# Kernel optimization log

Hardware: AMD Instinct MI355X
Metric: run time of the kernel (lower is better)

The kernel has to match this reference:

```python
import jax, jax.numpy as jnp
import numpy as np

B, N, D, H, E, FF = 4, 256, 256, 8, 32, 512
DK = D // H
SCALE = DK ** -0.5
NEG = -9.0e15


def _norm_mul(t, w, b, ms):
    # graph norm over node axis (dim=1)
    mean = jnp.mean(t, axis=1, keepdims=True)
    std = jnp.sqrt(jnp.mean((t - ms * mean) ** 2, axis=1, keepdims=True))
    return w * (t - ms * mean) / (std + 1e-6) + b


def _layer_norm(t, w, b):
    mu = jnp.mean(t, axis=-1, keepdims=True)
    var = jnp.mean((t - mu) ** 2, axis=-1, keepdims=True)
    return w * (t - mu) * jax.lax.rsqrt(var + 1e-5) + b


def _ffn(t, W1, b1, W2, b2):
    return jax.nn.gelu(t @ W1 + b1, approximate=False) @ W2 + b2


def _forward(x, edge_fea, attn_bias, params, adj, adj1, use_adj):
    (gn1_w, gn1_b, gn1_ms, ln1_w, ln1_b, Wq, bq, Wk, bk, Wv, bv,
     Wap, bap, Wep, bep, Wo, bo, Woe, gn2_w, gn2_b, gn2_ms,
     W1, b1, W2, b2, ln2_w, ln2_b, W1e, b1e, W2e, b2e) = params
    adj_f = adj.astype(x.dtype)
    adj1_f = adj1.astype(x.dtype)

    y = _norm_mul(x, gn1_w, gn1_b, gn1_ms)              # [B,N,D]
    e_n = _layer_norm(edge_fea, ln1_w, ln1_b)           # [B,N,N,E]

    q = (y @ Wq + bq).reshape(B, N, H, DK) * SCALE
    k = (y @ Wk + bk).reshape(B, N, H, DK)
    v = (y @ Wv + bv).reshape(B, N, H, DK)
    scores = jnp.einsum('bihd,bjhd->bhij', q, k)        # [B,H,N,N]
    if use_adj:
        scores = jnp.where(adj_f[:, None] > 0, scores, NEG) * adj_f[:, None]

    # global branch: multiplicative attn_bias then softmax
    x_long = jax.nn.softmax(scores * attn_bias, axis=-1)
    out_long = jnp.einsum('bhij,bjhd->bihd', x_long, v)

    # edge-feature fusion
    edge_bias = jnp.swapaxes(e_n @ Wep + bep, 1, 3)     # [B,H,N,N]
    x_proj = (jnp.swapaxes(scores, 1, 3) @ Wap + bap) * adj1_f[..., None]  # [B,N,N,E]
    e_attn = (e_n + x_proj) @ Woe                       # [B,N,N,E]

    # local branch: scores gated by edge bias and local adjacency
    x_local = jax.nn.softmax(scores * edge_bias * adj1_f[:, None], axis=-1)
    out_local = jnp.einsum('bhij,bjhd->bihd', x_local, v)

    attn_out = (out_local + out_long).reshape(B, N, D) @ Wo + bo

    x_out = x + attn_out
    x_out = x_out + _ffn(_norm_mul(x_out, gn2_w, gn2_b, gn2_ms), W1, b1, W2, b2)

    e1 = edge_fea + e_attn
    e_out = e1 + _ffn(_layer_norm(e1, ln2_w, ln2_b), W1e, b1e, W2e, b2e)
    return x_out, e_out


def setup_inputs() -> dict:
    key = jax.random.key(0)
    keys = list(jax.random.split(key, 32))

    def nk():
        return keys.pop()

    def w(shape, s=0.02):
        return jax.random.normal(nk(), shape, jnp.float32) * s

    inp = {}
    inp['x'] = jax.random.normal(nk(), (B, N, D), jnp.float32)
    inp['adj'] = jax.random.randint(nk(), (B, N, N), 0, 2).astype(jnp.int32)
    inp['adj1'] = (jax.random.uniform(nk(), (B, N, N)) < 0.15).astype(jnp.int32)
    inp['use_adj'] = 1
    inp['edge_fea'] = jax.random.normal(nk(), (B, N, N, E), jnp.float32)
    inp['attn_bias'] = jax.random.uniform(nk(), (B, H, N, N), jnp.float32)
    for nm, dim in [('gn1', D), ('gn2', D)]:
        inp[nm + '_w'] = jnp.ones((dim,), jnp.float32)
        inp[nm + '_b'] = jnp.zeros((dim,), jnp.float32)
        inp[nm + '_ms'] = jnp.ones((dim,), jnp.float32)
    for nm, dim in [('ln1', E), ('ln2', E)]:
        inp[nm + '_w'] = jnp.ones((dim,), jnp.float32)
        inp[nm + '_b'] = jnp.zeros((dim,), jnp.float32)
    inp['Wq'], inp['bq'] = w((D, D)), jnp.zeros((D,), jnp.float32)
    inp['Wk'], inp['bk'] = w((D, D)), jnp.zeros((D,), jnp.float32)
    inp['Wv'], inp['bv'] = w((D, D)), jnp.zeros((D,), jnp.float32)
    inp['Wap'], inp['bap'] = w((H, E)), jnp.zeros((E,), jnp.float32)
    inp['Wep'], inp['bep'] = w((E, H)), jnp.zeros((H,), jnp.float32)
    inp['Wo'], inp['bo'] = w((D, D)), jnp.zeros((D,), jnp.float32)
    inp['Woe'] = w((E, E))
    inp['W1'], inp['b1'] = w((D, FF)), jnp.zeros((FF,), jnp.float32)
    inp['W2'], inp['b2'] = w((FF, D)), jnp.zeros((D,), jnp.float32)
    inp['W1e'], inp['b1e'] = w((E, FF)), jnp.zeros((FF,), jnp.float32)
    inp['W2e'], inp['b2e'] = w((FF, E)), jnp.zeros((E,), jnp.float32)
    return inp


def reference(x, adj, adj1, use_adj, edge_fea, attn_bias,
              gn1_w, gn1_b, gn1_ms, gn2_w, gn2_b, gn2_ms,
              ln1_w, ln1_b, ln2_w, ln2_b,
              Wq, bq, Wk, bk, Wv, bv, Wap, bap, Wep, bep, Wo, bo, Woe,
              W1, b1, W2, b2, W1e, b1e, W2e, b2e):
    params = (gn1_w, gn1_b, gn1_ms, ln1_w, ln1_b, Wq, bq, Wk, bk, Wv, bv,
              Wap, bap, Wep, bep, Wo, bo, Woe, gn2_w, gn2_b, gn2_ms,
              W1, b1, W2, b2, ln2_w, ln2_b, W1e, b1e, W2e, b2e)
    return _forward(x, edge_fea, attn_bias, params, adj, adj1, use_adj)
```

## Files before the change

kernel.cpp:

```cpp
#include <hip/hip_runtime.h>
#include <math.h>

constexpr int B_ = 4, N_ = 256, D_ = 256, H_ = 8, E_ = 32, FF_ = 512, DK_ = 32;
constexpr float SCALE_ = 0.17677669529663687f;
constexpr float NEG_ = -9.0e15f;

typedef unsigned short u16;
typedef unsigned int u32;
typedef __attribute__((ext_vector_type(8))) short bf16x8;
typedef __attribute__((ext_vector_type(4))) float f32x4;
typedef __attribute__((ext_vector_type(8))) _Float16 f16x8;
typedef __attribute__((ext_vector_type(2))) _Float16 f16x2;
typedef __attribute__((ext_vector_type(2))) __fp16 fp16x2_raw;

__device__ __forceinline__ float gelu_fast(float x) {
  float u = x * x;
  float q = x * fmaf(-0.071354816272f, u, -1.5957691216057308f);
  float e = __expf(q);
  return x * __builtin_amdgcn_rcpf(1.f + e);
}

__device__ __forceinline__ f16x2 cvt_pk_f16(float a, float b) {
  union { fp16x2_raw i; f16x2 o; } u;
  u.i = __builtin_amdgcn_cvt_pkrtz(a, b);
  return u.o;
}

__device__ __forceinline__ f16x2 gelu_pk(f16x2 x) {
  const f16x2 C5 = {(_Float16)0.0199471f, (_Float16)0.0199471f};
  const f16x2 C3 = {(_Float16)-0.1329807f, (_Float16)-0.1329807f};
  const f16x2 C1 = {(_Float16)0.7978846f, (_Float16)0.7978846f};
  const f16x2 HALF = {(_Float16)0.5f, (_Float16)0.5f};
  const f16x2 ONE = {(_Float16)1.f, (_Float16)1.f};
  f16x2 w = x * x;
  f16x2 p = w * C5 + C3;
  p = w * p + C1;
  f16x2 t = x * p + ONE;
  f16x2 hx = x * HALF;
  return hx * t;
}

__device__ __forceinline__ u16 f2bf(float x) {
  union { float f; u32 u; } v; v.f = x;
  u32 r = v.u + 0x7fffu + ((v.u >> 16) & 1u);
  return (u16)(r >> 16);
}

__device__ __forceinline__ u32 pk2bf(float a, float b) {
  union { float f; u32 u; } x, y; x.f = a; y.f = b;
  u32 ra = (x.u + 0x7fffu + ((x.u >> 16) & 1u)) >> 16;
  u32 rb = (y.u + 0x7fffu + ((y.u >> 16) & 1u)) & 0xffff0000u;
  return ra | rb;
}

__device__ __forceinline__ float bf2f(u16 h) {
  union { u32 u; float f; } v; v.u = ((u32)h) << 16; return v.f;
}

__global__ __launch_bounds__(256) void front_kernel(
    const float* __restrict__ Wq, const float* __restrict__ Wk,
    const float* __restrict__ Wv, const float* __restrict__ Wo,
    const float* __restrict__ W1, const float* __restrict__ W2,
    const float* __restrict__ W1e, const float* __restrict__ W2e,
    const float* __restrict__ Woe, const float* __restrict__ Wap,
    const float* __restrict__ bap,
    u16* __restrict__ wxp, u16* __restrict__ w1p, u16* __restrict__ w2p,
    u16* __restrict__ woep, u16* __restrict__ wwp,
    const float* __restrict__ x, float2* __restrict__ part,
    const float* __restrict__ e_in, const float* __restrict__ lnw,
    const float* __restrict__ lnb, const float* __restrict__ Wep,
    const float* __restrict__ bep, const int* __restrict__ adj1,
    u16* __restrict__ e_nb, u16* __restrict__ eb16) {
  int bx = blockIdx.x;
  int tid = threadIdx.x;
  if (bx < 256) {
    int idx = bx * 256 + tid;
    const float* W;
    int rel, Nn, kcs, cmask;
    if (idx < 32768) {
      int m = idx >> 13;
      W = (m == 0) ? Wq : (m == 1) ? Wk : (m == 2) ? Wv : Wo;
      rel = idx & 8191; Nn = 256; kcs = 4; cmask = 15;
    } else if (idx < 49152) {
      W = W1; rel = idx - 32768; Nn = 512; kcs = 5; cmask = 31;
    } else {
      W = W2; rel = idx - 49152; Nn = 256; kcs = 4; cmask = 15;
    }
    int fr = rel >> 6, lane = rel & 63;
    int kc = fr >> kcs, ctt = fr & cmask;
    int krow = kc * 32 + ((lane >> 4) << 3);
    int col = ctt * 16 + (lane & 15);
    u16 out[8];
#pragma unroll
    for (int j = 0; j < 8; j++)
      out[j] = f2bf(W[(size_t)(krow + j) * Nn + col]);
    uint4* dst = (uint4*)(wxp + ((size_t)idx << 3));
    *dst = make_uint4(((u32)out[0]) | ((u32)out[1] << 16),
                      ((u32)out[2]) | ((u32)out[3] << 16),
                      ((u32)out[4]) | ((u32)out[5] << 16),
                      ((u32)out[6]) | ((u32)out[7] << 16));
  } else if (bx < 320) {
    int idx = (bx - 256) * 256 + tid;
    {
      int t = idx >> 9, rem = idx & 511, lane = rem >> 3, j = rem & 7;
      int k = ((lane >> 4) << 3) + j, col = (t << 4) + (lane & 15);
      w1p[idx] = f2bf(W1e[k * FF_ + col]);
    }
    {
      int f = idx >> 9, rem = idx & 511, lane = rem >> 3, j = rem & 7;
      int nc = f >> 2, kp = (f >> 1) & 1, ct = f & 1;
      int unit = nc * 64 + kp * 32 + 16 * (j >> 2) + 4 * (lane >> 4) + (j & 3);
      int col = ct * 16 + (lane & 15);
      union { _Float16 h; u16 u; } cv;
      cv.h = (_Float16)W2e[unit * E_ + col];
      w2p[idx] = cv.u;
    }
    if (idx < 1024) {
      int ct = idx >> 9, rem = idx & 511, lane = rem >> 3, j = rem & 7;
      int k = ((lane >> 4) << 3) + j, col = ct * 16 + (lane & 15);
      woep[idx] = f2bf(Woe[k * E_ + col]);
      float v = 0.f;
      if (k < 8) {
        for (int e = 0; e < 32; e++) v += Wap[k * E_ + e] * Woe[e * E_ + col];
      } else if (k == 8) {
        for (int e = 0; e < 32; e++) v += bap[e] * Woe[e * E_ + col];
      }
      wwp[idx] = f2bf(v);
    }
  } else if (bx < 448) {
    int i = bx - 320;
    int b = i & 3, by = (i >> 2) & 3, nz = i >> 4;
    int d = tid & 63, gn = tid >> 6;
    __shared__ float2 red[4][64];
    const float* xp = x + ((size_t)b * N_ * D_) + (size_t)(nz * 32 + gn * 8) * D_ + by * 64 + d;
    float s = 0.f, s2 = 0.f;
#pragma unroll
    for (int i2 = 0; i2 < 8; i2++) { float v = xp[(size_t)i2 * D_]; s += v; s2 += v * v; }
    red[gn][d] = make_float2(s, s2);
    __syncthreads();
    if (tid < 64) {
      float2 a = red[0][d], b2 = red[1][d], c = red[2][d], e = red[3][d];
      part[((b * 4 + by) * 8 + nz) * 64 + d] =
          make_float2(a.x + b2.x + c.x + e.x, a.y + b2.y + c.y + e.y);
    }
  } else {
    size_t t = (size_t)(bx - 448) * 256 + tid;
    int b = (int)(t >> 16), n2 = (int)((t >> 8) & 255), n1 = (int)(t & 255);
    size_t rowid = ((size_t)(b * N_ + n1)) * N_ + n2;
    const float4* ip = (const float4*)(e_in + rowid * E_);
    float4 v[8];
    float s = 0.f;
#pragma unroll
    for (int i = 0; i < 8; i++) { v[i] = ip[i]; s += v[i].x + v[i].y + v[i].z + v[i].w; }
    float mu = s * (1.f / E_);
    float q = 0.f;
#pragma unroll
    for (int i = 0; i < 8; i++) {
      float a = v[i].x - mu, b2 = v[i].y - mu, c = v[i].z - mu, dd = v[i].w - mu;
      q += a * a + b2 * b2 + c * c + dd * dd;
    }
    float inv = rsqrtf(q * (1.f / E_) + 1e-5f);
    float ov[32];
#pragma unroll
    for (int i = 0; i < 8; i++) {
      float4 wv = ((const float4*)lnw)[i];
      float4 bv = ((const float4*)lnb)[i];
      ov[4 * i + 0] = wv.x * (v[i].x - mu) * inv + bv.x;
      ov[4 * i + 1] = wv.y * (v[i].y - mu) * inv + bv.y;
      ov[4 * i + 2] = wv.z * (v[i].z - mu) * inv + bv.z;
      ov[4 * i + 3] = wv.w * (v[i].w - mu) * inv + bv.w;
    }
    u32 pk[16];
#pragma unroll
    for (int i = 0; i < 16; i++) pk[i] = pk2bf(ov[2 * i], ov[2 * i + 1]);
    uint4* op = (uint4*)(e_nb + rowid * E_);
    op[0] = make_uint4(pk[0], pk[1], pk[2], pk[3]);
    op[1] = make_uint4(pk[4], pk[5], pk[6], pk[7]);
    op[2] = make_uint4(pk[8], pk[9], pk[10], pk[11]);
    op[3] = make_uint4(pk[12], pk[13], pk[14], pk[15]);
    float acc[8];
#pragma unroll
    for (int h = 0; h < 8; h++) acc[h] = bep[h];
#pragma unroll
    for (int e = 0; e < 32; e++) {
      float re = ov[e];
#pragma unroll
      for (int h = 0; h < 8; h++) acc[h] = fmaf(re, Wep[e * 8 + h], acc[h]);
    }
    float a1f = (float)adj1[t];
#pragma unroll
    for (int h = 0; h < 8; h++)
      eb16[(((size_t)b * H_ + h) * N_ + n2) * N_ + n1] = f2bf(acc[h] * a1f);
  }
}

__global__ __launch_bounds__(256) void gnorm_part_kernel(
    const float* __restrict__ x, float2* __restrict__ part) {
  int b = blockIdx.x, by = blockIdx.y, nz = blockIdx.z;
  int tid = threadIdx.x, d = tid & 63, gn = tid >> 6;
  __shared__ float2 red[4][64];
  const float* xp = x + ((size_t)b * N_ * D_) + (size_t)(nz * 32 + gn * 8) * D_ + by * 64 + d;
  float s = 0.f, s2 = 0.f;
#pragma unroll
  for (int i = 0; i < 8; i++) { float v = xp[(size_t)i * D_]; s += v; s2 += v * v; }
  red[gn][d] = make_float2(s, s2);
  __syncthreads();
  if (tid < 64) {
    float2 a = red[0][d], b2 = red[1][d], c = red[2][d], e = red[3][d];
    part[((b * 4 + by) * 8 + nz) * 64 + d] =
        make_float2(a.x + b2.x + c.x + e.x, a.y + b2.y + c.y + e.y);
  }
}

__global__ __launch_bounds__(256) void gnorm_apply_kernel(
    const float* __restrict__ x, const float* __restrict__ w,
    const float* __restrict__ bw, const float* __restrict__ ms,
    const float2* __restrict__ part, float* __restrict__ out) {
  int b = blockIdx.x, by = blockIdx.y, nz = blockIdx.z;
  int tid = threadIdx.x, d = tid & 63, gn = tid >> 6;
  int d0 = by * 64;
  float s = 0.f, s2 = 0.f;
#pragma unroll
  for (int i = 0; i < 8; i++) {
    float2 p = part[((b * 4 + by) * 8 + i) * 64 + d];
    s += p.x; s2 += p.y;
  }
  float mean = s * (1.f / N_);
  float m2 = ms[d0 + d] * mean;
  float var = fmaxf(s2 * (1.f / N_) - 2.f * m2 * mean + m2 * m2, 0.f);
  float inv = 1.f / (sqrtf(var) + 1e-6f);
  float W = w[d0 + d], Bb = bw[d0 + d];
  const float* xp = x + ((size_t)b * N_ * D_) + (size_t)(nz * 32 + gn * 8) * D_ + d0 + d;
  float* op = out + ((size_t)b * N_ * D_) + (size_t)(nz * 32 + gn * 8) * D_ + d0 + d;
#pragma unroll
  for (int i = 0; i < 8; i++)
    op[(size_t)i * D_] = W * (xp[(size_t)i * D_] - m2) * inv + Bb;
}

template <int GELU>
__global__ __launch_bounds__(256) void mgemm_kernel(
    const float* __restrict__ A, const u16* __restrict__ Wp,
    const float* __restrict__ bias, const float* __restrict__ res,
    float* __restrict__ C, int K, int Nn, float scale) {
  int tid = threadIdx.x;
  int w = tid >> 6, l = tid & 63;
  int rt = w & 1, cts = (w >> 1) << 1;
  int row0 = blockIdx.y * 32, col0 = blockIdx.x * 64;
  int nf = Nn >> 4;
  f32x4 acc[2];
#pragma unroll
  for (int c2 = 0; c2 < 2; c2++) {
    float bb = bias[col0 + (cts + c2) * 16 + (l & 15)];
    acc[c2] = (f32x4){bb, bb, bb, bb};
  }
  int arow = row0 + rt * 16 + (l & 15);
  const float* ap = A + (size_t)arow * K + ((l >> 4) << 3);
  int nkc = K >> 5;
  for (int kc = 0; kc < nkc; kc++) {
    float4 a0 = *(const float4*)(ap + kc * 32);
    float4 a1 = *(const float4*)(ap + kc * 32 + 4);
    union { bf16x8 v; u32 u[4]; } af;
    af.u[0] = pk2bf(a0.x, a0.y); af.u[1] = pk2bf(a0.z, a0.w);
    af.u[2] = pk2bf(a1.x, a1.y); af.u[3] = pk2bf(a1.z, a1.w);
#pragma unroll
    for (int c2 = 0; c2 < 2; c2++) {
      bf16x8 wf = *(const bf16x8*)(Wp + (((size_t)kc * nf + (col0 >> 4) + cts + c2) << 9) + (l << 3));
      acc[c2] = __builtin_amdgcn_mfma_f32_16x16x32_bf16(af.v, wf, acc[c2], 0, 0, 0);
    }
  }
#pragma unroll
  for (int c2 = 0; c2 < 2; c2++) {
    int col = col0 + (cts + c2) * 16 + (l & 15);
#pragma unroll
    for (int rr = 0; rr < 4; rr++) {
      int row = row0 + rt * 16 + (l >> 4) * 4 + rr;
      float v = acc[c2][rr] * scale;
      if (GELU) v = gelu_fast(v);
      if (res) v += res[(size_t)row * Nn + col];
      C[(size_t)row * Nn + col] = v;
    }
  }
}

__global__ __launch_bounds__(256) void qkv_mfma_kernel(
    const float* __restrict__ A, const u16* __restrict__ wxp,
    const float* __restrict__ bq, const float* __restrict__ bk,
    const float* __restrict__ bv,
    float* __restrict__ q, float* __restrict__ k, float* __restrict__ v) {
  int z = blockIdx.z;
  const u16* Wp = wxp + (size_t)z * 65536;
  const float* bias = (z == 0) ? bq : (z == 1) ? bk : bv;
  float* C = (z == 0) ? q : (z == 1) ? k : v;
  float scale = (z == 0) ? SCALE_ : 1.f;
  int tid = threadIdx.x;
  int w = tid >> 6, l = tid & 63;
  int rt = w & 1, cts = (w >> 1) << 1;
  int row0 = blockIdx.y * 32, col0 = blockIdx.x * 64;
  f32x4 acc[2];
#pragma unroll
  for (int c2 = 0; c2 < 2; c2++) {
    float bb = bias[col0 + (cts + c2) * 16 + (l & 15)];
    acc[c2] = (f32x4){bb, bb, bb, bb};
  }
  int arow = row0 + rt * 16 + (l & 15);
  const float* ap = A + (size_t)arow * D_ + ((l >> 4) << 3);
#pragma unroll
  for (int kc = 0; kc < 8; kc++) {
    float4 a0 = *(const float4*)(ap + kc * 32);
    float4 a1 = *(const float4*)(ap + kc * 32 + 4);
    union { bf16x8 v; u32 u[4]; } af;
    af.u[0] = pk2bf(a0.x, a0.y); af.u[1] = pk2bf(a0.z, a0.w);
    af.u[2] = pk2bf(a1.x, a1.y); af.u[3] = pk2bf(a1.z, a1.w);
#pragma unroll
    for (int c2 = 0; c2 < 2; c2++) {
      bf16x8 wf = *(const bf16x8*)(Wp + (((size_t)kc * 16 + (col0 >> 4) + cts + c2) << 9) + (l << 3));
      acc[c2] = __builtin_amdgcn_mfma_f32_16x16x32_bf16(af.v, wf, acc[c2], 0, 0, 0);
    }
  }
#pragma unroll
  for (int c2 = 0; c2 < 2; c2++) {
    int col = col0 + (cts + c2) * 16 + (l & 15);
#pragma unroll
    for (int rr = 0; rr < 4; rr++) {
      int row = row0 + rt * 16 + (l >> 4) * 4 + rr;
      C[(size_t)row * D_ + col] = acc[c2][rr] * scale;
    }
  }
}

__global__ __launch_bounds__(256) void scores_attn_kernel(
    const float* __restrict__ q, const float* __restrict__ k,
    const float* __restrict__ v, const int* __restrict__ adj,
    const int* __restrict__ use_adj, const float* __restrict__ ab,
    const u16* __restrict__ eb16,
    u16* __restrict__ scoresT, float* __restrict__ out) {
  int it2 = blockIdx.x, h = blockIdx.y, b = blockIdx.z;
  int tid = threadIdx.x;
  __shared__ float qt[16][33];
  __shared__ u16 sc[16][260];
  __shared__ float vst[32][260];
  __shared__ float psw[4][256];

  float kreg[32];
  {
    const float4* kp = (const float4*)(k + ((size_t)b * N_ + tid) * D_ + h * DK_);
#pragma unroll
    for (int i = 0; i < 8; i++) {
      float4 kv = kp[i];
      kreg[4 * i] = kv.x; kreg[4 * i + 1] = kv.y;
      kreg[4 * i + 2] = kv.z; kreg[4 * i + 3] = kv.w;
    }
  }
  for (int i2 = 0; i2 < 2; i2++) {
    int f = tid + (i2 << 8);
    int rr = f >> 5, d = f & 31;
    qt[rr][d] = q[((size_t)b * N_ + it2 * 16 + rr) * D_ + h * DK_ + d];
  }
  for (int i2 = 0; i2 < 32; i2++) {
    int f = tid + (i2 << 8);
    int j = f >> 5, d = f & 31;
    vst[d][j] = v[((size_t)b * N_ + j) * D_ + h * DK_ + d];
  }
  __syncthreads();

  int ua = use_adj[0];
  u32 sbuf[8];
  float sprev = 0.f;
#pragma unroll
  for (int r = 0; r < 16; r++) {
    float s = 0.f;
#pragma unroll
    for (int d = 0; d < 32; d++) s = fmaf(qt[r][d], kreg[d], s);
    int i = it2 * 16 + r;
    if (ua) {
      int a = adj[((size_t)b * N_ + i) * N_ + tid];
      s = (a > 0 ? s : NEG_) * (float)a;
    }
    sc[r][tid] = f2bf(s);
    if (r & 1) sbuf[r >> 1] = pk2bf(sprev, s); else sprev = s;
  }
  uint4* stp = (uint4*)(scoresT + ((((size_t)(b * N_ + tid)) * 8 + h) << 8) + (it2 << 4));
  stp[0] = make_uint4(sbuf[0], sbuf[1], sbuf[2], sbuf[3]);
  stp[1] = make_uint4(sbuf[4], sbuf[5], sbuf[6], sbuf[7]);
  __syncthreads();

  int w = tid >> 6, l = tid & 63;
  int d = l & 31, hf = l >> 5;
  for (int rr = 0; rr < 4; rr++) {
    int lr = w * 4 + rr;
    int i = it2 * 16 + lr;
    size_t base = (((size_t)b * H_ + h) * N_ + i) * N_ + l * 4;
    uint2 sB = *(const uint2*)&sc[lr][l * 4];
    float s4x = bf2f((u16)(sB.x & 0xffff)), s4y = bf2f((u16)(sB.x >> 16));
    float s4z = bf2f((u16)(sB.y & 0xffff)), s4w = bf2f((u16)(sB.y >> 16));
    uint2 eB = *(const uint2*)(eb16 + base);
    float e4x = bf2f((u16)(eB.x & 0xffff)), e4y = bf2f((u16)(eB.x >> 16));
    float e4z = bf2f((u16)(eB.y & 0xffff)), e4w = bf2f((u16)(eB.y >> 16));
    float4 a4 = *(const float4*)(ab + base);
    float sl[4] = {s4x * a4.x, s4y * a4.y, s4z * a4.z, s4w * a4.w};
    float scv[4] = {s4x * e4x, s4y * e4y, s4z * e4z, s4w * e4w};
    float ml = fmaxf(fmaxf(sl[0], sl[1]), fmaxf(sl[2], sl[3]));
    float mc = fmaxf(fmaxf(scv[0], scv[1]), fmaxf(scv[2], scv[3]));
#pragma unroll
    for (int o = 32; o; o >>= 1) { ml = fmaxf(ml, __shfl_xor(ml, o)); mc = fmaxf(mc, __shfl_xor(mc, o)); }
    float el[4], ec[4];
#pragma unroll
    for (int c = 0; c < 4; c++) { el[c] = __expf(sl[c] - ml); ec[c] = __expf(scv[c] - mc); }
    float suml = el[0] + el[1] + el[2] + el[3];
    float sumc = ec[0] + ec[1] + ec[2] + ec[3];
#pragma unroll
    for (int o = 32; o; o >>= 1) { suml += __shfl_xor(suml, o); sumc += __shfl_xor(sumc, o); }
    float rl = __builtin_amdgcn_rcpf(suml), rc = __builtin_amdgcn_rcpf(sumc);
    float4 p;
    p.x = el[0] * rl + ec[0] * rc; p.y = el[1] * rl + ec[1] * rc;
    p.z = el[2] * rl + ec[2] * rc; p.w = el[3] * rl + ec[3] * rc;
    *(float4*)&psw[w][l * 4] = p;
    float acc = 0.f;
#pragma unroll
    for (int jq = 0; jq < 32; jq++) {
      int j4 = hf * 128 + jq * 4;
      float4 pp = *(const float4*)&psw[w][j4];
      float4 vv = *(const float4*)&vst[d][j4];
      acc = fmaf(pp.x, vv.x, acc); acc = fmaf(pp.y, vv.y, acc);
      acc = fmaf(pp.z, vv.z, acc); acc = fmaf(pp.w, vv.w, acc);
    }
    acc += __shfl_xor(acc, 32);
    if (l < 32) out[((size_t)b * N_ + i) * D_ + h * DK_ + d] = acc;
  }
}

__global__ __launch_bounds__(256) void e_fused_kernel(
    const u16* __restrict__ e_nb, const u16* __restrict__ scoresT,
    const int* __restrict__ adj1, const u16* __restrict__ wwp,
    const float* __restrict__ edge_fea,
    const u16* __restrict__ woep, const float* __restrict__ lw,
    const float* __restrict__ lb, const u16* __restrict__ w1p,
    const float* __restrict__ b1e, const u16* __restrict__ w2p,
    const float* __restrict__ b2e, float* __restrict__ e_out) {
  __shared__ float e1s[4][32][36];
  __shared__ float stats[4][2][32];
  int tid = threadIdx.x;
  int w = tid >> 6, l = tid & 63;
  size_t row0 = (size_t)blockIdx.x * 128 + (size_t)w * 32;
  int kb = (l >> 4) * 8;

  bf16x8 wf0 = *(const bf16x8*)(woep + l * 8);
  bf16x8 wf1 = *(const bf16x8*)(woep + 512 + l * 8);
  bf16x8 wwf0 = *(const bf16x8*)(wwp + l * 8);
  bf16x8 wwf1 = *(const bf16x8*)(wwp + 512 + l * 8);
  f32x4 zero = (f32x4){0.f, 0.f, 0.f, 0.f};
  f32x4 eo[2][2];
#pragma unroll
  for (int rt = 0; rt < 2; rt++) {
    size_t gr = row0 + rt * 16 + (l & 15);
    int a1 = adj1[gr];
    bf16x8 enf = *(const bf16x8*)(e_nb + gr * 32 + kb);
    bf16x8 sf = (bf16x8){0, 0, 0, 0, 0, 0, 0, 0};
    int kg = l >> 4;
    if (kg == 0) {
      const u16* sp = scoresT + ((size_t)(gr >> 8) * 8) * 256 + (gr & 255);
#pragma unroll
      for (int hh = 0; hh < 8; hh++)
        sf[hh] = a1 ? (short)sp[hh * 256] : (short)0;
    } else if (kg == 1) {
      sf[0] = a1 ? (short)0x3F80 : (short)0;
    }
    f32x4 acc0 = __builtin_amdgcn_mfma_f32_16x16x32_bf16(sf, wwf0, zero, 0, 0, 0);
    f32x4 acc1 = __builtin_amdgcn_mfma_f32_16x16x32_bf16(sf, wwf1, zero, 0, 0, 0);
    eo[rt][0] = __builtin_amdgcn_mfma_f32_16x16x32_bf16(enf, wf0, acc0, 0, 0, 0);
    eo[rt][1] = __builtin_amdgcn_mfma_f32_16x16x32_bf16(enf, wf1, acc1, 0, 0, 0);
  }
#pragma unroll
  for (int rt = 0; rt < 2; rt++)
#pragma unroll
    for (int ct = 0; ct < 2; ct++) {
      int col = ct * 16 + (l & 15);
#pragma unroll
      for (int rr = 0; rr < 4; rr++) {
        int row = rt * 16 + (l >> 4) * 4 + rr;
        float ed = edge_fea[(row0 + row) * E_ + col];
        e1s[w][row][col] = ed + eo[rt][ct][rr];
      }
    }

  {
    int r = l >> 1, ch = (l & 1) * 16;
    float4 v0 = *(const float4*)&e1s[w][r][ch + 0];
    float4 v1 = *(const float4*)&e1s[w][r][ch + 4];
    float4 v2 = *(const float4*)&e1s[w][r][ch + 8];
    float4 v3 = *(const float4*)&e1s[w][r][ch + 12];
    float s = v0.x + v0.y + v0.z + v0.w + v1.x + v1.y + v1.z + v1.w +
              v2.x + v2.y + v2.z + v2.w + v3.x + v3.y + v3.z + v3.w;
    s += __shfl_xor(s, 1);
    float mu = s * (1.f / E_);
    float tmp[16] = {v0.x, v0.y, v0.z, v0.w, v1.x, v1.y, v1.z, v1.w,
                     v2.x, v2.y, v2.z, v2.w, v3.x, v3.y, v3.z, v3.w};
    float q = 0.f;
#pragma unroll
    for (int i = 0; i < 16; i++) { float dd = tmp[i] - mu; q += dd * dd; }
    q += __shfl_xor(q, 1);
    float inv = rsqrtf(q * (1.f / E_) + 1e-5f);
    stats[w][0][r] = mu;
    stats[w][1][r] = inv;
  }

  bf16x8 at[2];
  {
    float4 lw0 = *(const float4*)(lw + kb), lw1 = *(const float4*)(lw + kb + 4);
    float4 lb0 = *(const float4*)(lb + kb), lb1 = *(const float4*)(lb + kb + 4);
    float lwv[8] = {lw0.x, lw0.y, lw0.z, lw0.w, lw1.x, lw1.y, lw1.z, lw1.w};
    float lbv[8] = {lb0.x, lb0.y, lb0.z, lb0.w, lb1.x, lb1.y, lb1.z, lb1.w};
#pragma unroll
    for (int rt = 0; rt < 2; rt++) {
      int ar = rt * 16 + (l & 15);
      float mu = stats[w][0][ar], inv = stats[w][1][ar];
      float4 e0 = *(const float4*)&e1s[w][ar][kb];
      float4 e1v = *(const float4*)&e1s[w][ar][kb + 4];
      float ev[8] = {e0.x, e0.y, e0.z, e0.w, e1v.x, e1v.y, e1v.z, e1v.w};
#pragma unroll
      for (int j = 0; j < 8; j++)
        at[rt][j] = (short)f2bf(lwv[j] * (ev[j] - mu) * inv + lbv[j]);
    }
  }

  f32x4 oacc[2][2];
#pragma unroll
  for (int ct = 0; ct < 2; ct++) {
    float bb = b2e[ct * 16 + (l & 15)];
#pragma unroll
    for (int rt = 0; rt < 2; rt++)
      oacc[rt][ct] = (f32x4){bb, bb, bb, bb};
  }

#pragma unroll 4
  for (int st = 0; st < 16; st++) {
    bf16x8 w1f0 = *(const bf16x8*)(w1p + (((size_t)st * 2 + 0) << 9) + (l << 3));
    bf16x8 w1f1 = *(const bf16x8*)(w1p + (((size_t)st * 2 + 1) << 9) + (l << 3));
    f16x8 w2f0 = *(const f16x8*)(w2p + (((size_t)st * 2 + 0) << 9) + (l << 3));
    f16x8 w2f1 = *(const f16x8*)(w2p + (((size_t)st * 2 + 1) << 9) + (l << 3));
    float4 b40 = *(const float4*)(b1e + st * 32 + ((l >> 4) << 2));
    float4 b41 = *(const float4*)(b1e + st * 32 + 16 + ((l >> 4) << 2));
    f32x4 hi0 = (f32x4){b40.x, b40.y, b40.z, b40.w};
    f32x4 hi1 = (f32x4){b41.x, b41.y, b41.z, b41.w};
    f32x4 ht00 = __builtin_amdgcn_mfma_f32_16x16x32_bf16(w1f0, at[0], hi0, 0, 0, 0);
    f32x4 ht01 = __builtin_amdgcn_mfma_f32_16x16x32_bf16(w1f0, at[1], hi0, 0, 0, 0);
    f32x4 ht10 = __builtin_amdgcn_mfma_f32_16x16x32_bf16(w1f1, at[0], hi1, 0, 0, 0);
    f32x4 ht11 = __builtin_amdgcn_mfma_f32_16x16x32_bf16(w1f1, at[1], hi1, 0, 0, 0);
    {
      union { f16x8 v; f16x2 h2[4]; } a8;
      a8.h2[0] = gelu_pk(cvt_pk_f16(ht00[0], ht00[1]));
      a8.h2[1] = gelu_pk(cvt_pk_f16(ht00[2], ht00[3]));
      a8.h2[2] = gelu_pk(cvt_pk_f16(ht10[0], ht10[1]));
      a8.h2[3] = gelu_pk(cvt_pk_f16(ht10[2], ht10[3]));
      oacc[0][0] = __builtin_amdgcn_mfma_f32_16x16x32_f16(a8.v, w2f0, oacc[0][0], 0, 0, 0);
      oacc[0][1] = __builtin_amdgcn_mfma_f32_16x16x32_f16(a8.v, w2f1, oacc[0][1], 0, 0, 0);
    }
    {
      union { f16x8 v; f16x2 h2[4]; } a8;
      a8.h2[0] = gelu_pk(cvt_pk_f16(ht01[0], ht01[1]));
      a8.h2[1] = gelu_pk(cvt_pk_f16(ht01[2], ht01[3]));
      a8.h2[2] = gelu_pk(cvt_pk_f16(ht11[0], ht11[1]));
      a8.h2[3] = gelu_pk(cvt_pk_f16(ht11[2], ht11[3]));
      oacc[1][0] = __builtin_amdgcn_mfma_f32_16x16x32_f16(a8.v, w2f0, oacc[1][0], 0, 0, 0);
      oacc[1][1] = __builtin_amdgcn_mfma_f32_16x16x32_f16(a8.v, w2f1, oacc[1][1], 0, 0, 0);
    }
  }

#pragma unroll
  for (int rt = 0; rt < 2; rt++)
#pragma unroll
    for (int ct = 0; ct < 2; ct++) {
      int col = ct * 16 + (l & 15);
#pragma unroll
      for (int r = 0; r < 4; r++) {
        int rl = rt * 16 + (l >> 4) * 4 + r;
        e_out[(row0 + rl) * E_ + col] = e1s[w][rl][col] + oacc[rt][ct][r];
      }
    }
}

extern "C" void kernel_launch(void* const* d_in, const int* in_sizes, int n_in,
                              void* d_out, int out_size, void* d_ws, size_t ws_size,
                              hipStream_t stream) {
  (void)in_sizes; (void)n_in; (void)out_size; (void)ws_size;
  const float* x        = (const float*)d_in[0];
  const int*   adj      = (const int*)d_in[1];
  const int*   adj1     = (const int*)d_in[2];
  const int*   use_adj  = (const int*)d_in[3];
  const float* edge_fea = (const float*)d_in[4];
  const float* attnb    = (const float*)d_in[5];
  const float* gn1_w = (const float*)d_in[6];
  const float* gn1_b = (const float*)d_in[7];
  const float* gn1_ms = (const float*)d_in[8];
  const float* gn2_w = (const float*)d_in[9];
  const float* gn2_b = (const float*)d_in[10];
  const float* gn2_ms = (const float*)d_in[11];
  const float* ln1_w = (const float*)d_in[12];
  const float* ln1_b = (const float*)d_in[13];
  const float* ln2_w = (const float*)d_in[14];
  const float* ln2_b = (const float*)d_in[15];
  const float* Wq = (const float*)d_in[16];
  const float* bq = (const float*)d_in[17];
  const float* Wk = (const float*)d_in[18];
  const float* bk = (const float*)d_in[19];
  const float* Wv = (const float*)d_in[20];
  const float* bv = (const float*)d_in[21];
  const float* Wap = (const float*)d_in[22];
  const float* bap = (const float*)d_in[23];
  const float* Wep = (const float*)d_in[24];
  const float* bep = (const float*)d_in[25];
  const float* Wo = (const float*)d_in[26];
  const float* bo = (const float*)d_in[27];
  const float* Woe = (const float*)d_in[28];
  const float* W1 = (const float*)d_in[29];
  const float* b1 = (const float*)d_in[30];
  const float* W2 = (const float*)d_in[31];
  const float* b2 = (const float*)d_in[32];
  const float* W1e = (const float*)d_in[33];
  const float* b1e = (const float*)d_in[34];
  const float* W2e = (const float*)d_in[35];
  const float* b2e = (const float*)d_in[36];

  float* ws = (float*)d_ws;
  float* y      = ws;
  float* q      = ws + 262144;
  float* k      = ws + 524288;
  float* v      = ws + 786432;
  float* outs   = ws + 1048576;
  float* x_t    = ws + 1310720;
  float* h1     = ws + 1572864;
  u16*   eb16   = (u16*)(ws + 4194304);
  u16*   e_nb   = (u16*)(ws + 6291456);
  u16*   scoresT= (u16*)(ws + 10485760);
  u16*   wbase  = (u16*)(ws + 11534336);
  u16*   w1p    = wbase;
  u16*   w2p    = wbase + 16384;
  u16*   woep   = wbase + 32768;
  u16*   wwp    = wbase + 33792;
  float2* gpart = (float2*)(ws + 11551744);
  u16*   wxp    = (u16*)(ws + 11568128);
  float* x_out  = (float*)d_out;
  float* e_out  = (float*)d_out + 262144;

  dim3 gN(B_, 4, 8);
  front_kernel<<<1472, 256, 0, stream>>>(Wq, Wk, Wv, Wo, W1, W2,
                                         W1e, W2e, Woe, Wap, bap,
                                         wxp, w1p, w2p, woep, wwp,
                                         x, gpart,
                                         edge_fea, ln1_w, ln1_b, Wep, bep, adj1,
                                         e_nb, eb16);
  gnorm_apply_kernel<<<gN, 256, 0, stream>>>(x, gn1_w, gn1_b, gn1_ms, gpart, y);
  qkv_mfma_kernel<<<dim3(4, 32, 3), 256, 0, stream>>>(y, wxp, bq, bk, bv, q, k, v);
  scores_attn_kernel<<<dim3(16, 8, 4), 256, 0, stream>>>(q, k, v, adj, use_adj,
                                                         attnb, eb16, scoresT, outs);
  mgemm_kernel<0><<<dim3(4, 32), 256, 0, stream>>>(outs, wxp + 196608, bo, x, x_t, 256, 256, 1.f);
  gnorm_part_kernel<<<gN, 256, 0, stream>>>(x_t, gpart);
  gnorm_apply_kernel<<<gN, 256, 0, stream>>>(x_t, gn2_w, gn2_b, gn2_ms, gpart, y);
  mgemm_kernel<1><<<dim3(8, 32), 256, 0, stream>>>(y, wxp + 262144, b1, nullptr, h1, 256, 512, 1.f);
  mgemm_kernel<0><<<dim3(4, 32), 256, 0, stream>>>(h1, wxp + 393216, b2, x_t, x_out, 512, 256, 1.f);
  e_fused_kernel<<<2048, 256, 0, stream>>>(e_nb, scoresT, adj1, wwp, edge_fea,
                                           woep, ln2_w, ln2_b, w1p, b1e, w2p, b2e, e_out);
}
```

Measured before the change: 113.9 us.

## Halve query rows per attention block and prefetch edge-FFN weights

The scores/attention kernel now handles 8 query rows per block instead of 16, which doubles the grid to 1024 blocks for more parallelism. Each block still loads the full K and V tiles, so that traffic is repeated twice as often. Separately, the edge FFN loop in e_fused_kernel now software-prefetches the next step's W1/W2 fragments and biases into registers. This hides load latency behind the MFMA work at the cost of more registers.

```diff
diff --git a/kernel.cpp b/kernel.cpp
--- a/kernel.cpp
+++ b/kernel.cpp
@@ -336,8 +336,8 @@
     u16* __restrict__ scoresT, float* __restrict__ out) {
   int it2 = blockIdx.x, h = blockIdx.y, b = blockIdx.z;
   int tid = threadIdx.x;
-  __shared__ float qt[16][33];
-  __shared__ u16 sc[16][260];
+  __shared__ float qt[8][33];
+  __shared__ u16 sc[8][260];
   __shared__ float vst[32][260];
   __shared__ float psw[4][256];
 
@@ -351,11 +351,7 @@
       kreg[4 * i + 2] = kv.z; kreg[4 * i + 3] = kv.w;
     }
   }
-  for (int i2 = 0; i2 < 2; i2++) {
-    int f = tid + (i2 << 8);
-    int rr = f >> 5, d = f & 31;
-    qt[rr][d] = q[((size_t)b * N_ + it2 * 16 + rr) * D_ + h * DK_ + d];
-  }
+  qt[tid >> 5][tid & 31] = q[((size_t)b * N_ + it2 * 8 + (tid >> 5)) * D_ + h * DK_ + (tid & 31)];
   for (int i2 = 0; i2 < 32; i2++) {
     int f = tid + (i2 << 8);
     int j = f >> 5, d = f & 31;
@@ -364,14 +360,14 @@
   __syncthreads();
 
   int ua = use_adj[0];
-  u32 sbuf[8];
+  u32 sbuf[4];
   float sprev = 0.f;
 #pragma unroll
-  for (int r = 0; r < 16; r++) {
+  for (int r = 0; r < 8; r++) {
     float s = 0.f;
 #pragma unroll
     for (int d = 0; d < 32; d++) s = fmaf(qt[r][d], kreg[d], s);
-    int i = it2 * 16 + r;
+    int i = it2 * 8 + r;
     if (ua) {
       int a = adj[((size_t)b * N_ + i) * N_ + tid];
       s = (a > 0 ? s : NEG_) * (float)a;
@@ -379,16 +375,15 @@
     sc[r][tid] = f2bf(s);
     if (r & 1) sbuf[r >> 1] = pk2bf(sprev, s); else sprev = s;
   }
-  uint4* stp = (uint4*)(scoresT + ((((size_t)(b * N_ + tid)) * 8 + h) << 8) + (it2 << 4));
-  stp[0] = make_uint4(sbuf[0], sbuf[1], sbuf[2], sbuf[3]);
-  stp[1] = make_uint4(sbuf[4], sbuf[5], sbuf[6], sbuf[7]);
+  *(uint4*)(scoresT + ((((size_t)(b * N_ + tid)) * 8 + h) << 8) + (it2 << 3)) =
+      make_uint4(sbuf[0], sbuf[1], sbuf[2], sbuf[3]);
   __syncthreads();
 
   int w = tid >> 6, l = tid & 63;
   int d = l & 31, hf = l >> 5;
-  for (int rr = 0; rr < 4; rr++) {
-    int lr = w * 4 + rr;
-    int i = it2 * 16 + lr;
+  for (int rr = 0; rr < 2; rr++) {
+    int lr = w * 2 + rr;
+    int i = it2 * 8 + lr;
     size_t base = (((size_t)b * H_ + h) * N_ + i) * N_ + l * 4;
     uint2 sB = *(const uint2*)&sc[lr][l * 4];
     float s4x = bf2f((u16)(sB.x & 0xffff)), s4y = bf2f((u16)(sB.x >> 16));
@@ -532,28 +527,36 @@
       oacc[rt][ct] = (f32x4){bb, bb, bb, bb};
   }
 
+  int lsh = l << 3, brow = (l >> 4) << 2;
+  bf16x8 w1c0 = *(const bf16x8*)(w1p + lsh);
+  bf16x8 w1c1 = *(const bf16x8*)(w1p + 512 + lsh);
+  f16x8 w2c0 = *(const f16x8*)(w2p + lsh);
+  f16x8 w2c1 = *(const f16x8*)(w2p + 512 + lsh);
+  float4 bc0 = *(const float4*)(b1e + brow);
+  float4 bc1 = *(const float4*)(b1e + 16 + brow);
 #pragma unroll 4
   for (int st = 0; st < 16; st++) {
-    bf16x8 w1f0 = *(const bf16x8*)(w1p + (((size_t)st * 2 + 0) << 9) + (l << 3));
-    bf16x8 w1f1 = *(const bf16x8*)(w1p + (((size_t)st * 2 + 1) << 9) + (l << 3));
-    f16x8 w2f0 = *(const f16x8*)(w2p + (((size_t)st * 2 + 0) << 9) + (l << 3));
-    f16x8 w2f1 = *(const f16x8*)(w2p + (((size_t)st * 2 + 1) << 9) + (l << 3));
-    float4 b40 = *(const float4*)(b1e + st * 32 + ((l >> 4) << 2));
-    float4 b41 = *(const float4*)(b1e + st * 32 + 16 + ((l >> 4) << 2));
-    f32x4 hi0 = (f32x4){b40.x, b40.y, b40.z, b40.w};
-    f32x4 hi1 = (f32x4){b41.x, b41.y, b41.z, b41.w};
-    f32x4 ht00 = __builtin_amdgcn_mfma_f32_16x16x32_bf16(w1f0, at[0], hi0, 0, 0, 0);
-    f32x4 ht01 = __builtin_amdgcn_mfma_f32_16x16x32_bf16(w1f0, at[1], hi0, 0, 0, 0);
-    f32x4 ht10 = __builtin_amdgcn_mfma_f32_16x16x32_bf16(w1f1, at[0], hi1, 0, 0, 0);
-    f32x4 ht11 = __builtin_amdgcn_mfma_f32_16x16x32_bf16(w1f1, at[1], hi1, 0, 0, 0);
+    int stn = st < 15 ? st + 1 : 15;
+    bf16x8 w1n0 = *(const bf16x8*)(w1p + (((size_t)stn * 2 + 0) << 9) + lsh);
+    bf16x8 w1n1 = *(const bf16x8*)(w1p + (((size_t)stn * 2 + 1) << 9) + lsh);
+    f16x8 w2n0 = *(const f16x8*)(w2p + (((size_t)stn * 2 + 0) << 9) + lsh);
+    f16x8 w2n1 = *(const f16x8*)(w2p + (((size_t)stn * 2 + 1) << 9) + lsh);
+    float4 bn0 = *(const float4*)(b1e + stn * 32 + brow);
+    float4 bn1 = *(const float4*)(b1e + stn * 32 + 16 + brow);
+    f32x4 hi0 = (f32x4){bc0.x, bc0.y, bc0.z, bc0.w};
+    f32x4 hi1 = (f32x4){bc1.x, bc1.y, bc1.z, bc1.w};
+    f32x4 ht00 = __builtin_amdgcn_mfma_f32_16x16x32_bf16(w1c0, at[0], hi0, 0, 0, 0);
+    f32x4 ht01 = __builtin_amdgcn_mfma_f32_16x16x32_bf16(w1c0, at[1], hi0, 0, 0, 0);
+    f32x4 ht10 = __builtin_amdgcn_mfma_f32_16x16x32_bf16(w1c1, at[0], hi1, 0, 0, 0);
+    f32x4 ht11 = __builtin_amdgcn_mfma_f32_16x16x32_bf16(w1c1, at[1], hi1, 0, 0, 0);
     {
       union { f16x8 v; f16x2 h2[4]; } a8;
       a8.h2[0] = gelu_pk(cvt_pk_f16(ht00[0], ht00[1]));
       a8.h2[1] = gelu_pk(cvt_pk_f16(ht00[2], ht00[3]));
       a8.h2[2] = gelu_pk(cvt_pk_f16(ht10[0], ht10[1]));
       a8.h2[3] = gelu_pk(cvt_pk_f16(ht10[2], ht10[3]));
-      oacc[0][0] = __builtin_amdgcn_mfma_f32_16x16x32_f16(a8.v, w2f0, oacc[0][0], 0, 0, 0);
-      oacc[0][1] = __builtin_amdgcn_mfma_f32_16x16x32_f16(a8.v, w2f1, oacc[0][1], 0, 0, 0);
+      oacc[0][0] = __builtin_amdgcn_mfma_f32_16x16x32_f16(a8.v, w2c0, oacc[0][0], 0, 0, 0);
+      oacc[0][1] = __builtin_amdgcn_mfma_f32_16x16x32_f16(a8.v, w2c1, oacc[0][1], 0, 0, 0);
     }
     {
       union { f16x8 v; f16x2 h2[4]; } a8;
@@ -561,9 +564,10 @@
       a8.h2[1] = gelu_pk(cvt_pk_f16(ht01[2], ht01[3]));
       a8.h2[2] = gelu_pk(cvt_pk_f16(ht11[0], ht11[1]));
       a8.h2[3] = gelu_pk(cvt_pk_f16(ht11[2], ht11[3]));
-      oacc[1][0] = __builtin_amdgcn_mfma_f32_16x16x32_f16(a8.v, w2f0, oacc[1][0], 0, 0, 0);
-      oacc[1][1] = __builtin_amdgcn_mfma_f32_16x16x32_f16(a8.v, w2f1, oacc[1][1], 0, 0, 0);
-    }
+      oacc[1][0] = __builtin_amdgcn_mfma_f32_16x16x32_f16(a8.v, w2c0, oacc[1][0], 0, 0, 0);
+      oacc[1][1] = __builtin_amdgcn_mfma_f32_16x16x32_f16(a8.v, w2c1, oacc[1][1], 0, 0, 0);
+    }
+    w1c0 = w1n0; w1c1 = w1n1; w2c0 = w2n0; w2c1 = w2n1; bc0 = bn0; bc1 = bn1;
   }
 
 #pragma unroll
@@ -651,7 +655,7 @@
                                          e_nb, eb16);
   gnorm_apply_kernel<<<gN, 256, 0, stream>>>(x, gn1_w, gn1_b, gn1_ms, gpart, y);
   qkv_mfma_kernel<<<dim3(4, 32, 3), 256, 0, stream>>>(y, wxp, bq, bk, bv, q, k, v);
-  scores_attn_kernel<<<dim3(16, 8, 4), 256, 0, stream>>>(q, k, v, adj, use_adj,
+  scores_attn_kernel<<<dim3(32, 8, 4), 256, 0, stream>>>(q, k, v, adj, use_adj,
                                                          attnb, eb16, scoresT, outs);
   mgemm_kernel<0><<<dim3(4, 32), 256, 0, stream>>>(outs, wxp + 196608, bo, x, x_t, 256, 256, 1.f);
   gnorm_part_kernel<<<gN, 256, 0, stream>>>(x_t, gpart);
```

After: 116.8 us. 1.03x slower.
